# Performance work log

Measured on AMD Instinct MI355X. Metric: run time of the kernel, lower is better.

Reference implementation:

```python
import jax, jax.numpy as jnp
import numpy as np

B, N, C = 2048, 128, 128
H = 4
NW = 64


def setup_inputs() -> dict:
    key = jax.random.key(0)
    ks = jax.random.split(key, 6)
    return {
        "x": jax.random.normal(ks[0], (B, N, C), dtype=jnp.float32),
        "mask": jax.random.normal(ks[1], (NW, N, N), dtype=jnp.float32),
        "qkv_w": jax.random.normal(ks[2], (3 * C, C), dtype=jnp.float32) * (C ** -0.5),
        "qkv_b": jax.random.normal(ks[3], (3 * C,), dtype=jnp.float32) * 0.02,
        "proj_w": jax.random.normal(ks[4], (C, C), dtype=jnp.float32) * (C ** -0.5),
        "proj_b": jax.random.normal(ks[5], (C,), dtype=jnp.float32) * 0.02,
    }


def reference(x, mask, qkv_w, qkv_b, proj_w, proj_b):
    b, n, c = x.shape
    h = H
    hd = c // h
    scale = hd ** -0.5
    # qkv projection: [B,N,3C] -> [3,B,H,N,hd]
    qkv = (x @ qkv_w.T + qkv_b).reshape(b, n, 3, h, hd).transpose(2, 0, 3, 1, 4)
    q, k, v = qkv[0], qkv[1], qkv[2]
    # scores [B,H,N,N]
    attn = jnp.einsum("bhnd,bhmd->bhnm", q, k) * scale
    nw = mask.shape[0]
    # add per-window mask: view as [B//nW, nW, H, N, N] + mask[None,:,None]
    attn = attn.reshape(b // nw, nw, h, n, n) + mask[None, :, None, :, :]
    attn = attn.reshape(b, h, n, n)
    attn = jax.nn.softmax(attn, axis=-1)
    out = jnp.einsum("bhnm,bhmd->bhnd", attn, v)
    out = out.transpose(0, 2, 1, 3).reshape(b, n, c)
    out = out @ proj_w.T + proj_b
    return out
```

## Files before the change

kernel.cpp:

```cpp
#include <hip/hip_runtime.h>

typedef __bf16 bf16x8 __attribute__((ext_vector_type(8)));
typedef __bf16 bf16x4 __attribute__((ext_vector_type(4)));
typedef float  f32x4  __attribute__((ext_vector_type(4)));

#define LDS_XO 0
#define LDS_Q  32768
#define LDS_K  65536
#define LDS_VT 98304
#define LDS_P  131072
#define LDS_TOTAL 147456

__device__ __forceinline__ int swz(int row, int colb) {
    return row * 256 + (colb ^ ((row & 7) << 4));
}

__global__ void prep_weights(const float* __restrict__ qkv_w,
                             const float* __restrict__ proj_w,
                             __bf16* __restrict__ wq, __bf16* __restrict__ wp) {
    int i = blockIdx.x * 256 + threadIdx.x;
    wq[i] = (__bf16)qkv_w[i];
    if (i < 16384) wp[i] = (__bf16)proj_w[i];
}

__global__ void __launch_bounds__(256, 1)
attn_fused(const float* __restrict__ x, const float* __restrict__ mask,
           const float* __restrict__ qkv_b, const float* __restrict__ proj_b,
           const __bf16* __restrict__ wq, const __bf16* __restrict__ wp,
           float* __restrict__ out) {
    extern __shared__ char smem[];
    const int b    = blockIdx.x;
    const int tid  = threadIdx.x;
    const int wave = tid >> 6;
    const int lane = tid & 63;
    const int l16  = lane & 15;
    const int lg   = lane >> 4;

    {
        const float* xb = x + (size_t)b * 16384;
        #pragma unroll
        for (int it = 0; it < 8; ++it) {
            int i   = it * 256 + tid;
            int row = i >> 4;
            int c8  = (i & 15) << 3;
            float4 f0 = *(const float4*)(xb + row * 128 + c8);
            float4 f1 = *(const float4*)(xb + row * 128 + c8 + 4);
            bf16x8 v;
            v[0] = (__bf16)f0.x; v[1] = (__bf16)f0.y; v[2] = (__bf16)f0.z; v[3] = (__bf16)f0.w;
            v[4] = (__bf16)f1.x; v[5] = (__bf16)f1.y; v[6] = (__bf16)f1.z; v[7] = (__bf16)f1.w;
            *(bf16x8*)(smem + LDS_XO + swz(row, c8 * 2)) = v;
        }
    }
    __syncthreads();

    const int j0 = wave * 96;
    #pragma unroll
    for (int pass = 0; pass < 2; ++pass) {
        f32x4 acc[6][4];
        #pragma unroll
        for (int jt = 0; jt < 6; ++jt)
            #pragma unroll
            for (int nt = 0; nt < 4; ++nt)
                acc[jt][nt] = {0.f, 0.f, 0.f, 0.f};
        #pragma unroll
        for (int kc = 0; kc < 4; ++kc) {
            bf16x8 afr[6];
            #pragma unroll
            for (int jt = 0; jt < 6; ++jt)
                afr[jt] = *(const bf16x8*)(wq + (j0 + jt * 16 + l16) * 128 + kc * 32 + lg * 8);
            bf16x8 bfr[4];
            #pragma unroll
            for (int nt = 0; nt < 4; ++nt)
                bfr[nt] = *(const bf16x8*)(smem + LDS_XO +
                            swz((pass * 4 + nt) * 16 + l16, (kc * 32 + lg * 8) * 2));
            #pragma unroll
            for (int jt = 0; jt < 6; ++jt)
                #pragma unroll
                for (int nt = 0; nt < 4; ++nt)
                    acc[jt][nt] = __builtin_amdgcn_mfma_f32_16x16x32_bf16(
                                      afr[jt], bfr[nt], acc[jt][nt], 0, 0, 0);
        }
        #pragma unroll
        for (int jt = 0; jt < 6; ++jt) {
            int jbase = j0 + jt * 16 + lg * 4;
            float4 bias = *(const float4*)(qkv_b + jbase);
            #pragma unroll
            for (int nt = 0; nt < 4; ++nt) {
                int n = (pass * 4 + nt) * 16 + l16;
                f32x4 a = acc[jt][nt];
                __bf16 e0 = (__bf16)(a[0] + bias.x);
                __bf16 e1 = (__bf16)(a[1] + bias.y);
                __bf16 e2 = (__bf16)(a[2] + bias.z);
                __bf16 e3 = (__bf16)(a[3] + bias.w);
                if (jbase < 128) {
                    bf16x4 v4 = {e0, e1, e2, e3};
                    *(bf16x4*)(smem + LDS_Q + swz(n, jbase * 2)) = v4;
                } else if (jbase < 256) {
                    bf16x4 v4 = {e0, e1, e2, e3};
                    *(bf16x4*)(smem + LDS_K + swz(n, (jbase - 128) * 2)) = v4;
                } else {
                    int d = jbase - 256;
                    *(__bf16*)(smem + LDS_VT + swz(d + 0, n * 2)) = e0;
                    *(__bf16*)(smem + LDS_VT + swz(d + 1, n * 2)) = e1;
                    *(__bf16*)(smem + LDS_VT + swz(d + 2, n * 2)) = e2;
                    *(__bf16*)(smem + LDS_VT + swz(d + 3, n * 2)) = e3;
                }
            }
        }
    }
    __syncthreads();

    const int h = wave;
    const float sc = 0.17677669529663687f;
    bf16x8 kfr[8];
    #pragma unroll
    for (int mt = 0; mt < 8; ++mt)
        kfr[mt] = *(const bf16x8*)(smem + LDS_K + swz(mt * 16 + l16, (h * 32 + lg * 8) * 2));
    bf16x8 vfr[2][4];
    #pragma unroll
    for (int dt = 0; dt < 2; ++dt)
        #pragma unroll
        for (int kc = 0; kc < 4; ++kc)
            vfr[dt][kc] = *(const bf16x8*)(smem + LDS_VT +
                            swz(h * 32 + dt * 16 + l16, (kc * 32 + lg * 8) * 2));

    const float* mwin = mask + (size_t)(b & 63) * 16384;
    char* pbase = smem + LDS_P + wave * 4096;

    for (int nt = 0; nt < 8; ++nt) {
        bf16x8 qfr = *(const bf16x8*)(smem + LDS_Q + swz(nt * 16 + l16, (h * 32 + lg * 8) * 2));
        f32x4 s[8];
        #pragma unroll
        for (int mt = 0; mt < 8; ++mt) {
            f32x4 z = {0.f, 0.f, 0.f, 0.f};
            s[mt] = __builtin_amdgcn_mfma_f32_16x16x32_bf16(qfr, kfr[mt], z, 0, 0, 0);
        }
        float mx[4] = {-1e30f, -1e30f, -1e30f, -1e30f};
        #pragma unroll
        for (int mt = 0; mt < 8; ++mt)
            #pragma unroll
            for (int r = 0; r < 4; ++r) {
                float v = s[mt][r] * sc + mwin[(nt * 16 + lg * 4 + r) * 128 + mt * 16 + l16];
                s[mt][r] = v;
                mx[r] = fmaxf(mx[r], v);
            }
        #pragma unroll
        for (int r = 0; r < 4; ++r) {
            float m = mx[r];
            m = fmaxf(m, __shfl_xor(m, 1));
            m = fmaxf(m, __shfl_xor(m, 2));
            m = fmaxf(m, __shfl_xor(m, 4));
            m = fmaxf(m, __shfl_xor(m, 8));
            mx[r] = m;
        }
        float sm[4] = {0.f, 0.f, 0.f, 0.f};
        #pragma unroll
        for (int mt = 0; mt < 8; ++mt)
            #pragma unroll
            for (int r = 0; r < 4; ++r) {
                float p = __expf(s[mt][r] - mx[r]);
                s[mt][r] = p;
                sm[r] += p;
            }
        #pragma unroll
        for (int r = 0; r < 4; ++r) {
            float t = sm[r];
            t += __shfl_xor(t, 1);
            t += __shfl_xor(t, 2);
            t += __shfl_xor(t, 4);
            t += __shfl_xor(t, 8);
            sm[r] = 1.f / t;
        }
        #pragma unroll
        for (int mt = 0; mt < 8; ++mt)
            #pragma unroll
            for (int r = 0; r < 4; ++r)
                *(__bf16*)(pbase + swz(lg * 4 + r, (mt * 16 + l16) * 2)) =
                    (__bf16)(s[mt][r] * sm[r]);
        bf16x8 pafr[4];
        #pragma unroll
        for (int kc = 0; kc < 4; ++kc)
            pafr[kc] = *(const bf16x8*)(pbase + swz(l16, (kc * 32 + lg * 8) * 2));
        #pragma unroll
        for (int dt = 0; dt < 2; ++dt) {
            f32x4 o = {0.f, 0.f, 0.f, 0.f};
            #pragma unroll
            for (int kc = 0; kc < 4; ++kc)
                o = __builtin_amdgcn_mfma_f32_16x16x32_bf16(pafr[kc], vfr[dt][kc], o, 0, 0, 0);
            #pragma unroll
            for (int r = 0; r < 4; ++r)
                *(__bf16*)(smem + LDS_XO +
                    swz(nt * 16 + lg * 4 + r, (h * 32 + dt * 16 + l16) * 2)) = (__bf16)o[r];
        }
    }
    __syncthreads();

    f32x4 facc[2][8];
    #pragma unroll
    for (int nt2 = 0; nt2 < 2; ++nt2)
        #pragma unroll
        for (int ct = 0; ct < 8; ++ct)
            facc[nt2][ct] = {0.f, 0.f, 0.f, 0.f};
    #pragma unroll
    for (int kc = 0; kc < 4; ++kc) {
        bf16x8 afr[2];
        #pragma unroll
        for (int nt2 = 0; nt2 < 2; ++nt2)
            afr[nt2] = *(const bf16x8*)(smem + LDS_XO +
                          swz((wave * 2 + nt2) * 16 + l16, (kc * 32 + lg * 8) * 2));
        bf16x8 bfr[8];
        #pragma unroll
        for (int ct = 0; ct < 8; ++ct)
            bfr[ct] = *(const bf16x8*)(wp + (ct * 16 + l16) * 128 + kc * 32 + lg * 8);
        #pragma unroll
        for (int nt2 = 0; nt2 < 2; ++nt2)
            #pragma unroll
            for (int ct = 0; ct < 8; ++ct)
                facc[nt2][ct] = __builtin_amdgcn_mfma_f32_16x16x32_bf16(
                                    afr[nt2], bfr[ct], facc[nt2][ct], 0, 0, 0);
    }
    float* ob = out + (size_t)b * 16384;
    #pragma unroll
    for (int ct = 0; ct < 8; ++ct) {
        float pb = proj_b[ct * 16 + l16];
        #pragma unroll
        for (int nt2 = 0; nt2 < 2; ++nt2) {
            int n0 = (wave * 2 + nt2) * 16 + lg * 4;
            #pragma unroll
            for (int r = 0; r < 4; ++r)
                ob[(n0 + r) * 128 + ct * 16 + l16] = facc[nt2][ct][r] + pb;
        }
    }
}

extern "C" void kernel_launch(void* const* d_in, const int* in_sizes, int n_in,
                              void* d_out, int out_size, void* d_ws, size_t ws_size,
                              hipStream_t stream) {
    const float* x      = (const float*)d_in[0];
    const float* mask   = (const float*)d_in[1];
    const float* qkv_w  = (const float*)d_in[2];
    const float* qkv_b  = (const float*)d_in[3];
    const float* proj_w = (const float*)d_in[4];
    const float* proj_b = (const float*)d_in[5];
    float* out = (float*)d_out;

    __bf16* wq = (__bf16*)d_ws;
    __bf16* wp = wq + 49152;

    prep_weights<<<192, 256, 0, stream>>>(qkv_w, proj_w, wq, wp);

    hipFuncSetAttribute((const void*)attn_fused,
                        hipFuncAttributeMaxDynamicSharedMemorySize, LDS_TOTAL);
    attn_fused<<<2048, 256, LDS_TOTAL, stream>>>(x, mask, qkv_b, proj_b, wq, wp, out);
}
```

Before: 466.8 us.

## Double waves per block and split QKV, attention and projection work across eight waves

Result: no change. 473.9 us (+1.5%).

```diff
diff --git a/kernel.cpp b/kernel.cpp
--- a/kernel.cpp
+++ b/kernel.cpp
@@ -14,6 +14,9 @@
 __device__ __forceinline__ int swz(int row, int colb) {
     return row * 256 + (colb ^ ((row & 7) << 4));
 }
+__device__ __forceinline__ int pswz(int row, int colb) {
+    return row * 128 + (colb ^ ((row & 7) << 4));
+}
 
 __global__ void prep_weights(const float* __restrict__ qkv_w,
                              const float* __restrict__ proj_w,
@@ -23,7 +26,7 @@
     if (i < 16384) wp[i] = (__bf16)proj_w[i];
 }
 
-__global__ void __launch_bounds__(256, 1)
+__global__ void __launch_bounds__(512, 2)
 attn_fused(const float* __restrict__ x, const float* __restrict__ mask,
            const float* __restrict__ qkv_b, const float* __restrict__ proj_b,
            const __bf16* __restrict__ wq, const __bf16* __restrict__ wp,
@@ -39,8 +42,8 @@
     {
         const float* xb = x + (size_t)b * 16384;
         #pragma unroll
-        for (int it = 0; it < 8; ++it) {
-            int i   = it * 256 + tid;
+        for (int it = 0; it < 4; ++it) {
+            int i   = it * 512 + tid;
             int row = i >> 4;
             int c8  = (i & 15) << 3;
             float4 f0 = *(const float4*)(xb + row * 128 + c8);
@@ -53,20 +56,20 @@
     }
     __syncthreads();
 
-    const int j0 = wave * 96;
+    const int j0 = wave * 48;
     #pragma unroll
     for (int pass = 0; pass < 2; ++pass) {
-        f32x4 acc[6][4];
-        #pragma unroll
-        for (int jt = 0; jt < 6; ++jt)
+        f32x4 acc[3][4];
+        #pragma unroll
+        for (int jt = 0; jt < 3; ++jt)
             #pragma unroll
             for (int nt = 0; nt < 4; ++nt)
                 acc[jt][nt] = {0.f, 0.f, 0.f, 0.f};
         #pragma unroll
         for (int kc = 0; kc < 4; ++kc) {
-            bf16x8 afr[6];
-            #pragma unroll
-            for (int jt = 0; jt < 6; ++jt)
+            bf16x8 afr[3];
+            #pragma unroll
+            for (int jt = 0; jt < 3; ++jt)
                 afr[jt] = *(const bf16x8*)(wq + (j0 + jt * 16 + l16) * 128 + kc * 32 + lg * 8);
             bf16x8 bfr[4];
             #pragma unroll
@@ -74,14 +77,14 @@
                 bfr[nt] = *(const bf16x8*)(smem + LDS_XO +
                             swz((pass * 4 + nt) * 16 + l16, (kc * 32 + lg * 8) * 2));
             #pragma unroll
-            for (int jt = 0; jt < 6; ++jt)
+            for (int jt = 0; jt < 3; ++jt)
                 #pragma unroll
                 for (int nt = 0; nt < 4; ++nt)
                     acc[jt][nt] = __builtin_amdgcn_mfma_f32_16x16x32_bf16(
                                       afr[jt], bfr[nt], acc[jt][nt], 0, 0, 0);
         }
         #pragma unroll
-        for (int jt = 0; jt < 6; ++jt) {
+        for (int jt = 0; jt < 3; ++jt) {
             int jbase = j0 + jt * 16 + lg * 4;
             float4 bias = *(const float4*)(qkv_b + jbase);
             #pragma unroll
@@ -110,7 +113,8 @@
     }
     __syncthreads();
 
-    const int h = wave;
+    const int h  = wave >> 1;
+    const int rh = wave & 1;
     const float sc = 0.17677669529663687f;
     bf16x8 kfr[8];
     #pragma unroll
@@ -125,9 +129,11 @@
                             swz(h * 32 + dt * 16 + l16, (kc * 32 + lg * 8) * 2));
 
     const float* mwin = mask + (size_t)(b & 63) * 16384;
-    char* pbase = smem + LDS_P + wave * 4096;
-
-    for (int nt = 0; nt < 8; ++nt) {
+    char* pbase = smem + LDS_P + wave * 2048;
+
+    #pragma unroll
+    for (int i = 0; i < 4; ++i) {
+        const int nt = rh * 4 + i;
         bf16x8 qfr = *(const bf16x8*)(smem + LDS_Q + swz(nt * 16 + l16, (h * 32 + lg * 8) * 2));
         f32x4 s[8];
         #pragma unroll
@@ -171,65 +177,63 @@
             t += __shfl_xor(t, 8);
             sm[r] = 1.f / t;
         }
-        #pragma unroll
-        for (int mt = 0; mt < 8; ++mt)
-            #pragma unroll
-            for (int r = 0; r < 4; ++r)
-                *(__bf16*)(pbase + swz(lg * 4 + r, (mt * 16 + l16) * 2)) =
-                    (__bf16)(s[mt][r] * sm[r]);
-        bf16x8 pafr[4];
-        #pragma unroll
-        for (int kc = 0; kc < 4; ++kc)
-            pafr[kc] = *(const bf16x8*)(pbase + swz(l16, (kc * 32 + lg * 8) * 2));
-        #pragma unroll
-        for (int dt = 0; dt < 2; ++dt) {
-            f32x4 o = {0.f, 0.f, 0.f, 0.f};
-            #pragma unroll
-            for (int kc = 0; kc < 4; ++kc)
-                o = __builtin_amdgcn_mfma_f32_16x16x32_bf16(pafr[kc], vfr[dt][kc], o, 0, 0, 0);
+        f32x4 o[2];
+        o[0] = {0.f, 0.f, 0.f, 0.f};
+        o[1] = {0.f, 0.f, 0.f, 0.f};
+        #pragma unroll
+        for (int hp = 0; hp < 2; ++hp) {
+            #pragma unroll
+            for (int mtl = 0; mtl < 4; ++mtl) {
+                int mt = hp * 4 + mtl;
+                #pragma unroll
+                for (int r = 0; r < 4; ++r)
+                    *(__bf16*)(pbase + pswz(lg * 4 + r, (mtl * 16 + l16) * 2)) =
+                        (__bf16)(s[mt][r] * sm[r]);
+            }
+            #pragma unroll
+            for (int q = 0; q < 2; ++q) {
+                int kc = hp * 2 + q;
+                bf16x8 pafr = *(const bf16x8*)(pbase + pswz(l16, (q * 32 + lg * 8) * 2));
+                #pragma unroll
+                for (int dt = 0; dt < 2; ++dt)
+                    o[dt] = __builtin_amdgcn_mfma_f32_16x16x32_bf16(
+                                pafr, vfr[dt][kc], o[dt], 0, 0, 0);
+            }
+        }
+        #pragma unroll
+        for (int dt = 0; dt < 2; ++dt)
             #pragma unroll
             for (int r = 0; r < 4; ++r)
                 *(__bf16*)(smem + LDS_XO +
-                    swz(nt * 16 + lg * 4 + r, (h * 32 + dt * 16 + l16) * 2)) = (__bf16)o[r];
-        }
+                    swz(nt * 16 + lg * 4 + r, (h * 32 + dt * 16 + l16) * 2)) = (__bf16)o[dt][r];
     }
     __syncthreads();
 
-    f32x4 facc[2][8];
-    #pragma unroll
-    for (int nt2 = 0; nt2 < 2; ++nt2)
-        #pragma unroll
-        for (int ct = 0; ct < 8; ++ct)
-            facc[nt2][ct] = {0.f, 0.f, 0.f, 0.f};
+    f32x4 facc[8];
+    #pragma unroll
+    for (int ct = 0; ct < 8; ++ct)
+        facc[ct] = {0.f, 0.f, 0.f, 0.f};
     #pragma unroll
     for (int kc = 0; kc < 4; ++kc) {
-        bf16x8 afr[2];
-        #pragma unroll
-        for (int nt2 = 0; nt2 < 2; ++nt2)
-            afr[nt2] = *(const bf16x8*)(smem + LDS_XO +
-                          swz((wave * 2 + nt2) * 16 + l16, (kc * 32 + lg * 8) * 2));
+        bf16x8 afr = *(const bf16x8*)(smem + LDS_XO +
+                        swz(wave * 16 + l16, (kc * 32 + lg * 8) * 2));
         bf16x8 bfr[8];
         #pragma unroll
         for (int ct = 0; ct < 8; ++ct)
             bfr[ct] = *(const bf16x8*)(wp + (ct * 16 + l16) * 128 + kc * 32 + lg * 8);
         #pragma unroll
-        for (int nt2 = 0; nt2 < 2; ++nt2)
-            #pragma unroll
-            for (int ct = 0; ct < 8; ++ct)
-                facc[nt2][ct] = __builtin_amdgcn_mfma_f32_16x16x32_bf16(
-                                    afr[nt2], bfr[ct], facc[nt2][ct], 0, 0, 0);
+        for (int ct = 0; ct < 8; ++ct)
+            facc[ct] = __builtin_amdgcn_mfma_f32_16x16x32_bf16(
+                           afr, bfr[ct], facc[ct], 0, 0, 0);
     }
     float* ob = out + (size_t)b * 16384;
     #pragma unroll
     for (int ct = 0; ct < 8; ++ct) {
         float pb = proj_b[ct * 16 + l16];
-        #pragma unroll
-        for (int nt2 = 0; nt2 < 2; ++nt2) {
-            int n0 = (wave * 2 + nt2) * 16 + lg * 4;
-            #pragma unroll
-            for (int r = 0; r < 4; ++r)
-                ob[(n0 + r) * 128 + ct * 16 + l16] = facc[nt2][ct][r] + pb;
-        }
+        int n0 = wave * 16 + lg * 4;
+        #pragma unroll
+        for (int r = 0; r < 4; ++r)
+            ob[(n0 + r) * 128 + ct * 16 + l16] = facc[ct][r] + pb;
     }
 }
 
@@ -251,5 +255,5 @@
 
     hipFuncSetAttribute((const void*)attn_fused,
                         hipFuncAttributeMaxDynamicSharedMemorySize, LDS_TOTAL);
-    attn_fused<<<2048, 256, LDS_TOTAL, stream>>>(x, mask, qkv_b, proj_b, wq, wp, out);
-}
+    attn_fused<<<2048, 512, LDS_TOTAL, stream>>>(x, mask, qkv_b, proj_b, wq, wp, out);
+}
```
